# Kernel optimization log

Measured on AMD Instinct MI355X. Metric: run time of the kernel, lower is better.

Reference implementation:

```python
import jax, jax.numpy as jnp
import numpy as np

DIM_V = 512
H = 8
EPS = 1e-5

def _layernorm(x, g, b):
    mu = jnp.mean(x, axis=-1, keepdims=True)
    var = jnp.var(x, axis=-1, keepdims=True)
    return (x - mu) * jax.lax.rsqrt(var + EPS) * g + b

def setup_inputs() -> dict:
    key = jax.random.key(0)
    ks = jax.random.split(key, 10)
    B, Nq, Nk, dq, dk, dv = 8, 1024, 1024, 512, 512, DIM_V
    def lin(k, fan_in, shape):
        bound = 1.0 / np.sqrt(fan_in)
        return jax.random.uniform(k, shape, jnp.float32, -bound, bound)
    return {
        "Q": jax.random.normal(ks[0], (B, Nq, dq), jnp.float32),
        "K": jax.random.normal(ks[1], (B, Nk, dk), jnp.float32),
        "Wq": lin(ks[2], dq, (dv, dq)), "bq": lin(ks[3], dq, (dv,)),
        "Wk": lin(ks[4], dk, (dv, dk)), "bk": lin(ks[5], dk, (dv,)),
        "Wv": lin(ks[6], dk, (dv, dk)), "bv": lin(ks[7], dk, (dv,)),
        "Wo": lin(ks[8], dv, (dv, dv)), "bo": lin(ks[9], dv, (dv,)),
        "g0": jnp.ones((dv,), jnp.float32), "beta0": jnp.zeros((dv,), jnp.float32),
        "g1": jnp.ones((dv,), jnp.float32), "beta1": jnp.zeros((dv,), jnp.float32),
    }

def reference(Q, K, Wq, bq, Wk, bk, Wv, bv, Wo, bo, g0, beta0, g1, beta1):
    B, Nq, _ = Q.shape
    Nk = K.shape[1]
    d_h = DIM_V // H
    Qp = Q @ Wq.T + bq            # [B,Nq,dv]
    Kp = K @ Wk.T + bk            # [B,Nk,dv]
    Vp = K @ Wv.T + bv            # [B,Nk,dv]
    # split heads along feature dim (matches torch split(dim_split,2)+cat(0))
    Qh = Qp.reshape(B, Nq, H, d_h).transpose(0, 2, 1, 3)  # [B,H,Nq,dh]
    Kh = Kp.reshape(B, Nk, H, d_h).transpose(0, 2, 1, 3)
    Vh = Vp.reshape(B, Nk, H, d_h).transpose(0, 2, 1, 3)
    # NOTE: original scales by sqrt(dim_V), the FULL model dim
    scores = jnp.einsum('bhnd,bhmd->bhnm', Qh, Kh) / jnp.sqrt(jnp.float32(DIM_V))
    A = jax.nn.softmax(scores, axis=-1)                   # [B,H,Nq,Nk]
    Oh = Qh + jnp.einsum('bhnm,bhmd->bhnd', A, Vh)        # residual on projected Q
    O = Oh.transpose(0, 2, 1, 3).reshape(B, Nq, DIM_V)
    O = _layernorm(O, g0, beta0)
    O = O + jax.nn.relu(O @ Wo.T + bo)
    O = _layernorm(O, g1, beta1)
    return O
```

## Files before the change

### kernel.cpp

```cpp
#include <hip/hip_runtime.h>
#include <hip/hip_bf16.h>

typedef __hip_bfloat16 bf16;
typedef short bf16x8 __attribute__((ext_vector_type(8)));
typedef float f32x4 __attribute__((ext_vector_type(4)));
typedef unsigned int u32;

static __device__ __forceinline__ float bfu2f(unsigned short u) { return __uint_as_float((u32)u << 16); }
static __device__ __forceinline__ u32 pack2(float a, float b) {
    return (u32)__bfloat16_as_ushort(__float2bfloat16(a))
         | ((u32)__bfloat16_as_ushort(__float2bfloat16(b)) << 16);
}
static __device__ __forceinline__ float wave_sum(float v) {
    #pragma unroll
    for (int off = 32; off > 0; off >>= 1) v += __shfl_xor(v, off);
    return v;
}

static __device__ __forceinline__ void gll16(const bf16* g, bf16* l) {
    __builtin_amdgcn_global_load_lds((const __attribute__((address_space(1))) void*)g,
                                     (__attribute__((address_space(3))) void*)l,
                                     16, 0, 0);
}

__global__ __launch_bounds__(256) void castall(const float* __restrict__ Q,  const float* __restrict__ K,
                                               const float* __restrict__ Wq, const float* __restrict__ Wk,
                                               const float* __restrict__ Wv, const float* __restrict__ Wo,
                                               bf16* __restrict__ dQ,  bf16* __restrict__ dK,
                                               bf16* __restrict__ dWq, bf16* __restrict__ dWk,
                                               bf16* __restrict__ dWv, bf16* __restrict__ dWo)
{
    const int b = blockIdx.x;
    const float* src; bf16* dst; size_t off;
    if (b < 1024)      { src = Q;  dst = dQ;  off = (size_t)b * 4096; }
    else if (b < 2048) { src = K;  dst = dK;  off = (size_t)(b - 1024) * 4096; }
    else {
        const int wb = b - 2048, wi = wb >> 6;
        off = (size_t)(wb & 63) * 4096;
        src = wi == 0 ? Wq : wi == 1 ? Wk : wi == 2 ? Wv : Wo;
        dst = wi == 0 ? dWq : wi == 1 ? dWk : wi == 2 ? dWv : dWo;
    }
    const size_t p = off + threadIdx.x * 16;
    const float4 v0 = *(const float4*)(src + p);
    const float4 v1 = *(const float4*)(src + p + 4);
    const float4 v2 = *(const float4*)(src + p + 8);
    const float4 v3 = *(const float4*)(src + p + 12);
    uint4 o0, o1;
    o0.x = pack2(v0.x, v0.y); o0.y = pack2(v0.z, v0.w);
    o0.z = pack2(v1.x, v1.y); o0.w = pack2(v1.z, v1.w);
    o1.x = pack2(v2.x, v2.y); o1.y = pack2(v2.z, v2.w);
    o1.z = pack2(v3.x, v3.y); o1.w = pack2(v3.z, v3.w);
    *(uint4*)(dst + p)     = o0;
    *(uint4*)(dst + p + 8) = o1;
}

__global__ __launch_bounds__(256) void gemm_qkv(const bf16* __restrict__ Aq, const bf16* __restrict__ Ak,
                                                const bf16* __restrict__ Wq, const bf16* __restrict__ Wk,
                                                const bf16* __restrict__ Wv,
                                                const float* __restrict__ bq, const float* __restrict__ bk,
                                                const float* __restrict__ bv,
                                                bf16* __restrict__ oQ, bf16* __restrict__ oK,
                                                bf16* __restrict__ oV)
{
    __shared__ bf16 As[128 * 32];
    __shared__ bf16 Bs[128 * 32];

    const int tid = threadIdx.x, lane = tid & 63, wave = tid >> 6;
    const int yy = blockIdx.y, wi = yy >> 2;
    const bf16* A     = wi == 0 ? Aq : Ak;
    const bf16* W     = wi == 0 ? Wq : wi == 1 ? Wk : Wv;
    const float* bias = wi == 0 ? bq : wi == 1 ? bk : bv;
    bf16* out         = wi == 0 ? oQ : wi == 1 ? oK : oV;
    const int mode    = wi == 2 ? 2 : 1;
    const int bm = blockIdx.x * 128;
    const int bn = (yy & 3) * 128;

    const int srow = tid >> 2;
    const int sg8  = (((tid & 3) ^ (srow & 3)) * 8);
    const int wm = (wave >> 1) * 64, wn = (wave & 1) * 64;
    const int fr = lane & 15, fq = lane >> 4;
    const int kqs = ((fq ^ (fr & 3)) * 8);

    f32x4 acc[4][4] = {};
    const bf16* Ap = A + (size_t)(bm + srow) * 512 + sg8;
    const bf16* Wp = W + (size_t)(bn + srow) * 512 + sg8;
    bf16* AsD = As + 8 * tid;
    bf16* BsD = Bs + 8 * tid;

    for (int k0 = 0; k0 < 512; k0 += 32) {
        __syncthreads();
        gll16(Ap + k0,                    AsD);
        gll16(Ap + k0 + (size_t)64 * 512, AsD + 2048);
        gll16(Wp + k0,                    BsD);
        gll16(Wp + k0 + (size_t)64 * 512, BsD + 2048);
        __syncthreads();

        bf16x8 fa[4], fb[4];
        #pragma unroll
        for (int i = 0; i < 4; i++) {
            fa[i] = *(const bf16x8*)(&As[(wm + 16 * i + fr) * 32 + kqs]);
            fb[i] = *(const bf16x8*)(&Bs[(wn + 16 * i + fr) * 32 + kqs]);
        }
        #pragma unroll
        for (int i = 0; i < 4; i++)
            #pragma unroll
            for (int j = 0; j < 4; j++)
                acc[i][j] = __builtin_amdgcn_mfma_f32_16x16x32_bf16(fa[i], fb[j], acc[i][j], 0, 0, 0);
    }

    const int r0 = fq * 4;
    #pragma unroll
    for (int i = 0; i < 4; i++) {
        #pragma unroll
        for (int j = 0; j < 4; j++) {
            const int col = bn + wn + 16 * j + fr;
            const float bv2 = bias[col];
            #pragma unroll
            for (int r = 0; r < 4; r++) {
                const int row = bm + wm + 16 * i + r0 + r;
                const float v = acc[i][j][r] + bv2;
                const int b = row >> 10, n = row & 1023;
                const int h = col >> 6,  d = col & 63;
                size_t idx;
                if (mode == 1) idx = ((size_t)(b * 8 + h) * 1024 + n) * 64 + d;
                else           idx = ((size_t)(b * 8 + h) * 64 + d) * 1024 + n;
                out[idx] = __float2bfloat16(v);
            }
        }
    }
}

__global__ __launch_bounds__(256) void gemm_o(const bf16* __restrict__ A,
                                              const bf16* __restrict__ W,
                                              const float* __restrict__ bias,
                                              bf16* __restrict__ out)
{
    __shared__ bf16 As[64 * 32];
    __shared__ bf16 Bs[128 * 32];

    const int tid = threadIdx.x, lane = tid & 63, wave = tid >> 6;
    const int bm = blockIdx.x * 64;
    const int bn = blockIdx.y * 128;

    const int srow = tid >> 2;
    const int sg8  = (((tid & 3) ^ (srow & 3)) * 8);
    const int wn = wave * 32;
    const int fr = lane & 15, fq = lane >> 4;
    const int kqs = ((fq ^ (fr & 3)) * 8);

    f32x4 acc[4][2] = {};
    const bf16* Ap = A + (size_t)(bm + srow) * 512 + sg8;
    const bf16* Wp = W + (size_t)(bn + srow) * 512 + sg8;
    bf16* AsD = As + 8 * tid;
    bf16* BsD = Bs + 8 * tid;

    for (int k0 = 0; k0 < 512; k0 += 32) {
        __syncthreads();
        gll16(Ap + k0,                    AsD);
        gll16(Wp + k0,                    BsD);
        gll16(Wp + k0 + (size_t)64 * 512, BsD + 2048);
        __syncthreads();

        bf16x8 fa[4], fb[2];
        #pragma unroll
        for (int i = 0; i < 4; i++)
            fa[i] = *(const bf16x8*)(&As[(16 * i + fr) * 32 + kqs]);
        #pragma unroll
        for (int j = 0; j < 2; j++)
            fb[j] = *(const bf16x8*)(&Bs[(wn + 16 * j + fr) * 32 + kqs]);
        #pragma unroll
        for (int i = 0; i < 4; i++)
            #pragma unroll
            for (int j = 0; j < 2; j++)
                acc[i][j] = __builtin_amdgcn_mfma_f32_16x16x32_bf16(fa[i], fb[j], acc[i][j], 0, 0, 0);
    }

    const int r0 = fq * 4;
    #pragma unroll
    for (int i = 0; i < 4; i++) {
        #pragma unroll
        for (int j = 0; j < 2; j++) {
            const int col = bn + wn + 16 * j + fr;
            const float bv = bias[col];
            #pragma unroll
            for (int r = 0; r < 4; r++) {
                const int row = bm + 16 * i + r0 + r;
                out[(size_t)row * 512 + col] = __float2bfloat16(acc[i][j][r] + bv);
            }
        }
    }
}

__global__ __launch_bounds__(256) void attn_mfma(const bf16* __restrict__ Qh,
                                                 const bf16* __restrict__ Kh,
                                                 const bf16* __restrict__ VhT,
                                                 bf16* __restrict__ Oc)
{
    __shared__ bf16 Ks[64 * 64];
    __shared__ bf16 Vs[64 * 64];
    __shared__ bf16 Ps[4][16 * 72];

    const int tid = threadIdx.x, lane = tid & 63, w = tid >> 6;
    const int bh = blockIdx.y;
    const int wq = blockIdx.x * 64 + w * 16;

    const bf16* Qb = Qh  + ((size_t)bh * 1024 + wq) * 64;
    const bf16* Kb = Kh  + (size_t)bh * 1024 * 64;
    const bf16* Vb = VhT + (size_t)bh * 64 * 1024;

    const int fl = lane & 15, fq = lane >> 4;
    const int flk = fl & 7;
    const int gA = (fq ^ flk) * 8;
    const int gB = ((4 | fq) ^ flk) * 8;

    bf16x8 qf0 = *(const bf16x8*)(Qb + fl * 64 + fq * 8);
    bf16x8 qf1 = *(const bf16x8*)(Qb + fl * 64 + 32 + fq * 8);

    f32x4 o[4] = {};
    float lsum = 0.f;
    const float sc2 = 0.04419417382415922f * 1.4426950408889634f;

    const int srow = tid >> 3;
    const int sg8  = (((tid & 7) ^ (srow & 7)) * 8);
    const bf16* KbR = Kb + (size_t)srow * 64 + sg8;
    const bf16* VbR0 = Vb + (size_t)srow * 1024 + sg8;
    const bf16* VbR1 = Vb + (size_t)(srow + 32) * 1024 + sg8;
    bf16* KsD = Ks + 8 * tid;
    bf16* VsD = Vs + 8 * tid;

    for (int kt = 0; kt < 16; kt++) {
        const int m0 = kt * 64;
        __syncthreads();
        gll16(KbR + (size_t)m0 * 64,        KsD);
        gll16(KbR + (size_t)(m0 + 32) * 64, KsD + 2048);
        gll16(VbR0 + m0,                    VsD);
        gll16(VbR1 + m0,                    VsD + 2048);
        __syncthreads();

        f32x4 st[4] = {};
        #pragma unroll
        for (int tm = 0; tm < 4; tm++) {
            bf16x8 kf0 = *(const bf16x8*)(&Ks[(16 * tm + fl) * 64 + gA]);
            bf16x8 kf1 = *(const bf16x8*)(&Ks[(16 * tm + fl) * 64 + gB]);
            st[tm] = __builtin_amdgcn_mfma_f32_16x16x32_bf16(kf0, qf0, st[tm], 0, 0, 0);
            st[tm] = __builtin_amdgcn_mfma_f32_16x16x32_bf16(kf1, qf1, st[tm], 0, 0, 0);
        }

        #pragma unroll
        for (int tm = 0; tm < 4; tm++) {
            float p0 = __builtin_amdgcn_exp2f(st[tm][0] * sc2);
            float p1 = __builtin_amdgcn_exp2f(st[tm][1] * sc2);
            float p2 = __builtin_amdgcn_exp2f(st[tm][2] * sc2);
            float p3 = __builtin_amdgcn_exp2f(st[tm][3] * sc2);
            lsum += (p0 + p1) + (p2 + p3);
            uint2 pk;
            pk.x = pack2(p0, p1);
            pk.y = pack2(p2, p3);
            *(uint2*)(&Ps[w][fl * 72 + 16 * tm + fq * 4]) = pk;
        }

        bf16x8 pf0 = *(const bf16x8*)(&Ps[w][fl * 72 + fq * 8]);
        bf16x8 pf1 = *(const bf16x8*)(&Ps[w][fl * 72 + 32 + fq * 8]);
        #pragma unroll
        for (int jd = 0; jd < 4; jd++) {
            bf16x8 vf0 = *(const bf16x8*)(&Vs[(16 * jd + fl) * 64 + gA]);
            bf16x8 vf1 = *(const bf16x8*)(&Vs[(16 * jd + fl) * 64 + gB]);
            o[jd] = __builtin_amdgcn_mfma_f32_16x16x32_bf16(vf0, pf0, o[jd], 0, 0, 0);
            o[jd] = __builtin_amdgcn_mfma_f32_16x16x32_bf16(vf1, pf1, o[jd], 0, 0, 0);
        }
    }

    lsum += __shfl_xor(lsum, 16);
    lsum += __shfl_xor(lsum, 32);
    const float linv = 1.f / lsum;

    const int b = bh >> 3, h = bh & 7;
    const size_t obase = ((size_t)(b * 1024 + wq + fl)) * 512 + h * 64;
    #pragma unroll
    for (int jd = 0; jd < 4; jd++) {
        const ushort4 qr = *(const ushort4*)(Qb + fl * 64 + 16 * jd + fq * 4);
        const float v0 = o[jd][0] * linv + bfu2f(qr.x);
        const float v1 = o[jd][1] * linv + bfu2f(qr.y);
        const float v2 = o[jd][2] * linv + bfu2f(qr.z);
        const float v3 = o[jd][3] * linv + bfu2f(qr.w);
        uint2 w2;
        w2.x = pack2(v0, v1);
        w2.y = pack2(v2, v3);
        *(uint2*)(&Oc[obase + 16 * jd + fq * 4]) = w2;
    }
}

__global__ __launch_bounds__(256) void ln0(const bf16* __restrict__ X,
                                           const float* __restrict__ g,
                                           const float* __restrict__ be,
                                           bf16* __restrict__ Y)
{
    const int lane = threadIdx.x & 63;
    const int row = blockIdx.x * 4 + (threadIdx.x >> 6);
    const size_t base = (size_t)row * 512 + lane * 8;
    const bf16x8 xv = *(const bf16x8*)(X + base);
    float x[8];
    #pragma unroll
    for (int j = 0; j < 8; j++) x[j] = bfu2f((unsigned short)xv[j]);
    float s = 0.f, s2 = 0.f;
    #pragma unroll
    for (int j = 0; j < 8; j++) { s += x[j]; s2 += x[j] * x[j]; }
    s = wave_sum(s); s2 = wave_sum(s2);
    const float mean = s * (1.f / 512.f);
    const float var = s2 * (1.f / 512.f) - mean * mean;
    const float rs = rsqrtf(fmaxf(var, 0.f) + 1e-5f);
    const float4 gv0 = *(const float4*)(g + lane * 8);
    const float4 gv1 = *(const float4*)(g + lane * 8 + 4);
    const float4 bv0 = *(const float4*)(be + lane * 8);
    const float4 bv1 = *(const float4*)(be + lane * 8 + 4);
    uint4 ov;
    ov.x = pack2((x[0]-mean)*rs*gv0.x + bv0.x, (x[1]-mean)*rs*gv0.y + bv0.y);
    ov.y = pack2((x[2]-mean)*rs*gv0.z + bv0.z, (x[3]-mean)*rs*gv0.w + bv0.w);
    ov.z = pack2((x[4]-mean)*rs*gv1.x + bv1.x, (x[5]-mean)*rs*gv1.y + bv1.y);
    ov.w = pack2((x[6]-mean)*rs*gv1.z + bv1.z, (x[7]-mean)*rs*gv1.w + bv1.w);
    *(uint4*)(Y + base) = ov;
}

__global__ __launch_bounds__(256) void ln1(const bf16* __restrict__ X,
                                           const bf16* __restrict__ R,
                                           const float* __restrict__ g,
                                           const float* __restrict__ be,
                                           float* __restrict__ Y)
{
    const int lane = threadIdx.x & 63;
    const int row = blockIdx.x * 4 + (threadIdx.x >> 6);
    const size_t base = (size_t)row * 512 + lane * 8;
    const bf16x8 xv = *(const bf16x8*)(X + base);
    const bf16x8 rv = *(const bf16x8*)(R + base);
    float x[8];
    #pragma unroll
    for (int j = 0; j < 8; j++)
        x[j] = bfu2f((unsigned short)rv[j]) + fmaxf(bfu2f((unsigned short)xv[j]), 0.f);
    float s = 0.f, s2 = 0.f;
    #pragma unroll
    for (int j = 0; j < 8; j++) { s += x[j]; s2 += x[j] * x[j]; }
    s = wave_sum(s); s2 = wave_sum(s2);
    const float mean = s * (1.f / 512.f);
    const float var = s2 * (1.f / 512.f) - mean * mean;
    const float rs = rsqrtf(fmaxf(var, 0.f) + 1e-5f);
    const float4 gv0 = *(const float4*)(g + lane * 8);
    const float4 gv1 = *(const float4*)(g + lane * 8 + 4);
    const float4 bv0 = *(const float4*)(be + lane * 8);
    const float4 bv1 = *(const float4*)(be + lane * 8 + 4);
    float4 y0, y1;
    y0.x = (x[0]-mean)*rs*gv0.x + bv0.x; y0.y = (x[1]-mean)*rs*gv0.y + bv0.y;
    y0.z = (x[2]-mean)*rs*gv0.z + bv0.z; y0.w = (x[3]-mean)*rs*gv0.w + bv0.w;
    y1.x = (x[4]-mean)*rs*gv1.x + bv1.x; y1.y = (x[5]-mean)*rs*gv1.y + bv1.y;
    y1.z = (x[6]-mean)*rs*gv1.z + bv1.z; y1.w = (x[7]-mean)*rs*gv1.w + bv1.w;
    *(float4*)(Y + base)     = y0;
    *(float4*)(Y + base + 4) = y1;
}

extern "C" void kernel_launch(void* const* d_in, const int* in_sizes, int n_in,
                              void* d_out, int out_size, void* d_ws, size_t ws_size,
                              hipStream_t stream)
{
    const float* Q   = (const float*)d_in[0];
    const float* K   = (const float*)d_in[1];
    const float* Wq  = (const float*)d_in[2];
    const float* bq  = (const float*)d_in[3];
    const float* Wk  = (const float*)d_in[4];
    const float* bk  = (const float*)d_in[5];
    const float* Wv  = (const float*)d_in[6];
    const float* bv  = (const float*)d_in[7];
    const float* Wo  = (const float*)d_in[8];
    const float* bo  = (const float*)d_in[9];
    const float* g0  = (const float*)d_in[10];
    const float* be0 = (const float*)d_in[11];
    const float* g1  = (const float*)d_in[12];
    const float* be1 = (const float*)d_in[13];
    float* out = (float*)d_out;

    const size_t NQK = (size_t)8 * 1024 * 512;
    const size_t NW  = (size_t)512 * 512;
    bf16* ws   = (bf16*)d_ws;
    bf16* cQ   = ws;
    bf16* cK   = cQ + NQK;
    bf16* cWq  = cK + NQK;
    bf16* cWk  = cWq + NW;
    bf16* cWv  = cWk + NW;
    bf16* cWo  = cWv + NW;
    bf16* pQh  = cWo + NW;
    bf16* pKh  = pQh + NQK;
    bf16* pVhT = pKh + NQK;
    bf16* pOc  = (bf16*)d_out;
    bf16* pO1  = pKh;
    bf16* pTmp = pQh;

    castall<<<2304, 256, 0, stream>>>(Q, K, Wq, Wk, Wv, Wo, cQ, cK, cWq, cWk, cWv, cWo);
    gemm_qkv<<<dim3(64, 12), 256, 0, stream>>>(cQ, cK, cWq, cWk, cWv, bq, bk, bv, pQh, pKh, pVhT);
    attn_mfma<<<dim3(16, 64), 256, 0, stream>>>(pQh, pKh, pVhT, pOc);
    ln0<<<2048, 256, 0, stream>>>(pOc, g0, be0, pO1);
    gemm_o<<<dim3(128, 4), 256, 0, stream>>>(pO1, cWo, bo, pTmp);
    ln1<<<2048, 256, 0, stream>>>(pTmp, pO1, g1, be1, out);
}
```

Before: 189.1 us.

## Double-buffer LDS tiles in QKV, output-projection and attention kernels

```diff
diff --git a/kernel.cpp b/kernel.cpp
--- a/kernel.cpp
+++ b/kernel.cpp
@@ -62,8 +62,8 @@
                                                 bf16* __restrict__ oQ, bf16* __restrict__ oK,
                                                 bf16* __restrict__ oV)
 {
-    __shared__ bf16 As[128 * 32];
-    __shared__ bf16 Bs[128 * 32];
+    __shared__ bf16 As[2][128 * 32];
+    __shared__ bf16 Bs[2][128 * 32];
 
     const int tid = threadIdx.x, lane = tid & 63, wave = tid >> 6;
     const int yy = blockIdx.y, wi = yy >> 2;
@@ -84,28 +84,35 @@
     f32x4 acc[4][4] = {};
     const bf16* Ap = A + (size_t)(bm + srow) * 512 + sg8;
     const bf16* Wp = W + (size_t)(bn + srow) * 512 + sg8;
-    bf16* AsD = As + 8 * tid;
-    bf16* BsD = Bs + 8 * tid;
-
+    const int ld = 8 * tid;
+
+    gll16(Ap,                    As[0] + ld);
+    gll16(Ap + (size_t)64 * 512, As[0] + 2048 + ld);
+    gll16(Wp,                    Bs[0] + ld);
+    gll16(Wp + (size_t)64 * 512, Bs[0] + 2048 + ld);
+
+    int cur = 0;
     for (int k0 = 0; k0 < 512; k0 += 32) {
         __syncthreads();
-        gll16(Ap + k0,                    AsD);
-        gll16(Ap + k0 + (size_t)64 * 512, AsD + 2048);
-        gll16(Wp + k0,                    BsD);
-        gll16(Wp + k0 + (size_t)64 * 512, BsD + 2048);
-        __syncthreads();
-
+        if (k0 + 32 < 512) {
+            const int nxt = cur ^ 1;
+            gll16(Ap + k0 + 32,                    As[nxt] + ld);
+            gll16(Ap + k0 + 32 + (size_t)64 * 512, As[nxt] + 2048 + ld);
+            gll16(Wp + k0 + 32,                    Bs[nxt] + ld);
+            gll16(Wp + k0 + 32 + (size_t)64 * 512, Bs[nxt] + 2048 + ld);
+        }
         bf16x8 fa[4], fb[4];
         #pragma unroll
         for (int i = 0; i < 4; i++) {
-            fa[i] = *(const bf16x8*)(&As[(wm + 16 * i + fr) * 32 + kqs]);
-            fb[i] = *(const bf16x8*)(&Bs[(wn + 16 * i + fr) * 32 + kqs]);
+            fa[i] = *(const bf16x8*)(&As[cur][(wm + 16 * i + fr) * 32 + kqs]);
+            fb[i] = *(const bf16x8*)(&Bs[cur][(wn + 16 * i + fr) * 32 + kqs]);
         }
         #pragma unroll
         for (int i = 0; i < 4; i++)
             #pragma unroll
             for (int j = 0; j < 4; j++)
                 acc[i][j] = __builtin_amdgcn_mfma_f32_16x16x32_bf16(fa[i], fb[j], acc[i][j], 0, 0, 0);
+        cur ^= 1;
     }
 
     const int r0 = fq * 4;
@@ -135,8 +142,8 @@
                                               const float* __restrict__ bias,
                                               bf16* __restrict__ out)
 {
-    __shared__ bf16 As[64 * 32];
-    __shared__ bf16 Bs[128 * 32];
+    __shared__ bf16 As[2][64 * 32];
+    __shared__ bf16 Bs[2][128 * 32];
 
     const int tid = threadIdx.x, lane = tid & 63, wave = tid >> 6;
     const int bm = blockIdx.x * 64;
@@ -151,28 +158,34 @@
     f32x4 acc[4][2] = {};
     const bf16* Ap = A + (size_t)(bm + srow) * 512 + sg8;
     const bf16* Wp = W + (size_t)(bn + srow) * 512 + sg8;
-    bf16* AsD = As + 8 * tid;
-    bf16* BsD = Bs + 8 * tid;
-
+    const int ld = 8 * tid;
+
+    gll16(Ap,                    As[0] + ld);
+    gll16(Wp,                    Bs[0] + ld);
+    gll16(Wp + (size_t)64 * 512, Bs[0] + 2048 + ld);
+
+    int cur = 0;
     for (int k0 = 0; k0 < 512; k0 += 32) {
         __syncthreads();
-        gll16(Ap + k0,                    AsD);
-        gll16(Wp + k0,                    BsD);
-        gll16(Wp + k0 + (size_t)64 * 512, BsD + 2048);
-        __syncthreads();
-
+        if (k0 + 32 < 512) {
+            const int nxt = cur ^ 1;
+            gll16(Ap + k0 + 32,                    As[nxt] + ld);
+            gll16(Wp + k0 + 32,                    Bs[nxt] + ld);
+            gll16(Wp + k0 + 32 + (size_t)64 * 512, Bs[nxt] + 2048 + ld);
+        }
         bf16x8 fa[4], fb[2];
         #pragma unroll
         for (int i = 0; i < 4; i++)
-            fa[i] = *(const bf16x8*)(&As[(16 * i + fr) * 32 + kqs]);
+            fa[i] = *(const bf16x8*)(&As[cur][(16 * i + fr) * 32 + kqs]);
         #pragma unroll
         for (int j = 0; j < 2; j++)
-            fb[j] = *(const bf16x8*)(&Bs[(wn + 16 * j + fr) * 32 + kqs]);
+            fb[j] = *(const bf16x8*)(&Bs[cur][(wn + 16 * j + fr) * 32 + kqs]);
         #pragma unroll
         for (int i = 0; i < 4; i++)
             #pragma unroll
             for (int j = 0; j < 2; j++)
                 acc[i][j] = __builtin_amdgcn_mfma_f32_16x16x32_bf16(fa[i], fb[j], acc[i][j], 0, 0, 0);
+        cur ^= 1;
     }
 
     const int r0 = fq * 4;
@@ -196,8 +209,8 @@
                                                  const bf16* __restrict__ VhT,
                                                  bf16* __restrict__ Oc)
 {
-    __shared__ bf16 Ks[64 * 64];
-    __shared__ bf16 Vs[64 * 64];
+    __shared__ bf16 Ks[2][64 * 64];
+    __shared__ bf16 Vs[2][64 * 64];
     __shared__ bf16 Ps[4][16 * 72];
 
     const int tid = threadIdx.x, lane = tid & 63, w = tid >> 6;
@@ -222,26 +235,33 @@
 
     const int srow = tid >> 3;
     const int sg8  = (((tid & 7) ^ (srow & 7)) * 8);
-    const bf16* KbR = Kb + (size_t)srow * 64 + sg8;
+    const bf16* KbR  = Kb + (size_t)srow * 64 + sg8;
     const bf16* VbR0 = Vb + (size_t)srow * 1024 + sg8;
     const bf16* VbR1 = Vb + (size_t)(srow + 32) * 1024 + sg8;
-    bf16* KsD = Ks + 8 * tid;
-    bf16* VsD = Vs + 8 * tid;
-
+    const int ld = 8 * tid;
+
+    gll16(KbR,               Ks[0] + ld);
+    gll16(KbR + 32 * 64,     Ks[0] + 2048 + ld);
+    gll16(VbR0,              Vs[0] + ld);
+    gll16(VbR1,              Vs[0] + 2048 + ld);
+
+    int cur = 0;
     for (int kt = 0; kt < 16; kt++) {
-        const int m0 = kt * 64;
         __syncthreads();
-        gll16(KbR + (size_t)m0 * 64,        KsD);
-        gll16(KbR + (size_t)(m0 + 32) * 64, KsD + 2048);
-        gll16(VbR0 + m0,                    VsD);
-        gll16(VbR1 + m0,                    VsD + 2048);
-        __syncthreads();
+        if (kt < 15) {
+            const int nxt = cur ^ 1;
+            const int m1 = (kt + 1) * 64;
+            gll16(KbR + (size_t)m1 * 64,        Ks[nxt] + ld);
+            gll16(KbR + (size_t)(m1 + 32) * 64, Ks[nxt] + 2048 + ld);
+            gll16(VbR0 + m1,                    Vs[nxt] + ld);
+            gll16(VbR1 + m1,                    Vs[nxt] + 2048 + ld);
+        }
 
         f32x4 st[4] = {};
         #pragma unroll
         for (int tm = 0; tm < 4; tm++) {
-            bf16x8 kf0 = *(const bf16x8*)(&Ks[(16 * tm + fl) * 64 + gA]);
-            bf16x8 kf1 = *(const bf16x8*)(&Ks[(16 * tm + fl) * 64 + gB]);
+            bf16x8 kf0 = *(const bf16x8*)(&Ks[cur][(16 * tm + fl) * 64 + gA]);
+            bf16x8 kf1 = *(const bf16x8*)(&Ks[cur][(16 * tm + fl) * 64 + gB]);
             st[tm] = __builtin_amdgcn_mfma_f32_16x16x32_bf16(kf0, qf0, st[tm], 0, 0, 0);
             st[tm] = __builtin_amdgcn_mfma_f32_16x16x32_bf16(kf1, qf1, st[tm], 0, 0, 0);
         }
@@ -263,11 +283,12 @@
         bf16x8 pf1 = *(const bf16x8*)(&Ps[w][fl * 72 + 32 + fq * 8]);
         #pragma unroll
         for (int jd = 0; jd < 4; jd++) {
-            bf16x8 vf0 = *(const bf16x8*)(&Vs[(16 * jd + fl) * 64 + gA]);
-            bf16x8 vf1 = *(const bf16x8*)(&Vs[(16 * jd + fl) * 64 + gB]);
+            bf16x8 vf0 = *(const bf16x8*)(&Vs[cur][(16 * jd + fl) * 64 + gA]);
+            bf16x8 vf1 = *(const bf16x8*)(&Vs[cur][(16 * jd + fl) * 64 + gB]);
             o[jd] = __builtin_amdgcn_mfma_f32_16x16x32_bf16(vf0, pf0, o[jd], 0, 0, 0);
             o[jd] = __builtin_amdgcn_mfma_f32_16x16x32_bf16(vf1, pf1, o[jd], 0, 0, 0);
         }
+        cur ^= 1;
     }
 
     lsum += __shfl_xor(lsum, 16);
```

Result: slower. 196.1 us (+3.7%).

## Drop LDS staging in GEMMs and attention, load MFMA fragments directly from global

Applied to the files above, without the earlier changes.

```diff
diff --git a/kernel.cpp b/kernel.cpp
--- a/kernel.cpp
+++ b/kernel.cpp
@@ -15,12 +15,6 @@
     #pragma unroll
     for (int off = 32; off > 0; off >>= 1) v += __shfl_xor(v, off);
     return v;
-}
-
-static __device__ __forceinline__ void gll16(const bf16* g, bf16* l) {
-    __builtin_amdgcn_global_load_lds((const __attribute__((address_space(1))) void*)g,
-                                     (__attribute__((address_space(3))) void*)l,
-                                     16, 0, 0);
 }
 
 __global__ __launch_bounds__(256) void castall(const float* __restrict__ Q,  const float* __restrict__ K,
@@ -62,9 +56,6 @@
                                                 bf16* __restrict__ oQ, bf16* __restrict__ oK,
                                                 bf16* __restrict__ oV)
 {
-    __shared__ bf16 As[128 * 32];
-    __shared__ bf16 Bs[128 * 32];
-
     const int tid = threadIdx.x, lane = tid & 63, wave = tid >> 6;
     const int yy = blockIdx.y, wi = yy >> 2;
     const bf16* A     = wi == 0 ? Aq : Ak;
@@ -75,31 +66,20 @@
     const int bm = blockIdx.x * 128;
     const int bn = (yy & 3) * 128;
 
-    const int srow = tid >> 2;
-    const int sg8  = (((tid & 3) ^ (srow & 3)) * 8);
     const int wm = (wave >> 1) * 64, wn = (wave & 1) * 64;
     const int fr = lane & 15, fq = lane >> 4;
-    const int kqs = ((fq ^ (fr & 3)) * 8);
 
     f32x4 acc[4][4] = {};
-    const bf16* Ap = A + (size_t)(bm + srow) * 512 + sg8;
-    const bf16* Wp = W + (size_t)(bn + srow) * 512 + sg8;
-    bf16* AsD = As + 8 * tid;
-    bf16* BsD = Bs + 8 * tid;
-
+    const bf16* Ap = A + (size_t)(bm + wm + fr) * 512 + fq * 8;
+    const bf16* Wp = W + (size_t)(bn + wn + fr) * 512 + fq * 8;
+
+    #pragma unroll 2
     for (int k0 = 0; k0 < 512; k0 += 32) {
-        __syncthreads();
-        gll16(Ap + k0,                    AsD);
-        gll16(Ap + k0 + (size_t)64 * 512, AsD + 2048);
-        gll16(Wp + k0,                    BsD);
-        gll16(Wp + k0 + (size_t)64 * 512, BsD + 2048);
-        __syncthreads();
-
         bf16x8 fa[4], fb[4];
         #pragma unroll
         for (int i = 0; i < 4; i++) {
-            fa[i] = *(const bf16x8*)(&As[(wm + 16 * i + fr) * 32 + kqs]);
-            fb[i] = *(const bf16x8*)(&Bs[(wn + 16 * i + fr) * 32 + kqs]);
+            fa[i] = *(const bf16x8*)(Ap + (size_t)(16 * i) * 512 + k0);
+            fb[i] = *(const bf16x8*)(Wp + (size_t)(16 * i) * 512 + k0);
         }
         #pragma unroll
         for (int i = 0; i < 4; i++)
@@ -135,39 +115,25 @@
                                               const float* __restrict__ bias,
                                               bf16* __restrict__ out)
 {
-    __shared__ bf16 As[64 * 32];
-    __shared__ bf16 Bs[128 * 32];
-
     const int tid = threadIdx.x, lane = tid & 63, wave = tid >> 6;
     const int bm = blockIdx.x * 64;
     const int bn = blockIdx.y * 128;
-
-    const int srow = tid >> 2;
-    const int sg8  = (((tid & 3) ^ (srow & 3)) * 8);
     const int wn = wave * 32;
     const int fr = lane & 15, fq = lane >> 4;
-    const int kqs = ((fq ^ (fr & 3)) * 8);
 
     f32x4 acc[4][2] = {};
-    const bf16* Ap = A + (size_t)(bm + srow) * 512 + sg8;
-    const bf16* Wp = W + (size_t)(bn + srow) * 512 + sg8;
-    bf16* AsD = As + 8 * tid;
-    bf16* BsD = Bs + 8 * tid;
-
+    const bf16* Ap = A + (size_t)(bm + fr) * 512 + fq * 8;
+    const bf16* Wp = W + (size_t)(bn + wn + fr) * 512 + fq * 8;
+
+    #pragma unroll 2
     for (int k0 = 0; k0 < 512; k0 += 32) {
-        __syncthreads();
-        gll16(Ap + k0,                    AsD);
-        gll16(Wp + k0,                    BsD);
-        gll16(Wp + k0 + (size_t)64 * 512, BsD + 2048);
-        __syncthreads();
-
         bf16x8 fa[4], fb[2];
         #pragma unroll
         for (int i = 0; i < 4; i++)
-            fa[i] = *(const bf16x8*)(&As[(16 * i + fr) * 32 + kqs]);
+            fa[i] = *(const bf16x8*)(Ap + (size_t)(16 * i) * 512 + k0);
         #pragma unroll
         for (int j = 0; j < 2; j++)
-            fb[j] = *(const bf16x8*)(&Bs[(wn + 16 * j + fr) * 32 + kqs]);
+            fb[j] = *(const bf16x8*)(Wp + (size_t)(16 * j) * 512 + k0);
         #pragma unroll
         for (int i = 0; i < 4; i++)
             #pragma unroll
@@ -196,22 +162,18 @@
                                                  const bf16* __restrict__ VhT,
                                                  bf16* __restrict__ Oc)
 {
-    __shared__ bf16 Ks[64 * 64];
-    __shared__ bf16 Vs[64 * 64];
     __shared__ bf16 Ps[4][16 * 72];
 
     const int tid = threadIdx.x, lane = tid & 63, w = tid >> 6;
-    const int bh = blockIdx.y;
-    const int wq = blockIdx.x * 64 + w * 16;
+    const int id = blockIdx.x;
+    const int bh = (id & 7) * 8 + (id >> 7);
+    const int wq = ((id >> 3) & 15) * 64 + w * 16;
 
     const bf16* Qb = Qh  + ((size_t)bh * 1024 + wq) * 64;
     const bf16* Kb = Kh  + (size_t)bh * 1024 * 64;
     const bf16* Vb = VhT + (size_t)bh * 64 * 1024;
 
     const int fl = lane & 15, fq = lane >> 4;
-    const int flk = fl & 7;
-    const int gA = (fq ^ flk) * 8;
-    const int gB = ((4 | fq) ^ flk) * 8;
 
     bf16x8 qf0 = *(const bf16x8*)(Qb + fl * 64 + fq * 8);
     bf16x8 qf1 = *(const bf16x8*)(Qb + fl * 64 + 32 + fq * 8);
@@ -220,30 +182,32 @@
     float lsum = 0.f;
     const float sc2 = 0.04419417382415922f * 1.4426950408889634f;
 
-    const int srow = tid >> 3;
-    const int sg8  = (((tid & 7) ^ (srow & 7)) * 8);
-    const bf16* KbR = Kb + (size_t)srow * 64 + sg8;
-    const bf16* VbR0 = Vb + (size_t)srow * 1024 + sg8;
-    const bf16* VbR1 = Vb + (size_t)(srow + 32) * 1024 + sg8;
-    bf16* KsD = Ks + 8 * tid;
-    bf16* VsD = Vs + 8 * tid;
+    const bf16* KpA = Kb + (size_t)fl * 64 + fq * 8;
+    const bf16* VpA = Vb + (size_t)fl * 1024 + fq * 8;
 
     for (int kt = 0; kt < 16; kt++) {
         const int m0 = kt * 64;
-        __syncthreads();
-        gll16(KbR + (size_t)m0 * 64,        KsD);
-        gll16(KbR + (size_t)(m0 + 32) * 64, KsD + 2048);
-        gll16(VbR0 + m0,                    VsD);
-        gll16(VbR1 + m0,                    VsD + 2048);
-        __syncthreads();
-
+
+        bf16x8 kf[4][2];
+        #pragma unroll
+        for (int tm = 0; tm < 4; tm++) {
+            const bf16* p = KpA + (size_t)(m0 + 16 * tm) * 64;
+            kf[tm][0] = *(const bf16x8*)(p);
+            kf[tm][1] = *(const bf16x8*)(p + 32);
+        }
         f32x4 st[4] = {};
         #pragma unroll
         for (int tm = 0; tm < 4; tm++) {
-            bf16x8 kf0 = *(const bf16x8*)(&Ks[(16 * tm + fl) * 64 + gA]);
-            bf16x8 kf1 = *(const bf16x8*)(&Ks[(16 * tm + fl) * 64 + gB]);
-            st[tm] = __builtin_amdgcn_mfma_f32_16x16x32_bf16(kf0, qf0, st[tm], 0, 0, 0);
-            st[tm] = __builtin_amdgcn_mfma_f32_16x16x32_bf16(kf1, qf1, st[tm], 0, 0, 0);
+            st[tm] = __builtin_amdgcn_mfma_f32_16x16x32_bf16(kf[tm][0], qf0, st[tm], 0, 0, 0);
+            st[tm] = __builtin_amdgcn_mfma_f32_16x16x32_bf16(kf[tm][1], qf1, st[tm], 0, 0, 0);
+        }
+
+        bf16x8 vf[4][2];
+        #pragma unroll
+        for (int jd = 0; jd < 4; jd++) {
+            const bf16* p = VpA + (size_t)(16 * jd) * 1024 + m0;
+            vf[jd][0] = *(const bf16x8*)(p);
+            vf[jd][1] = *(const bf16x8*)(p + 32);
         }
 
         #pragma unroll
@@ -263,10 +227,8 @@
         bf16x8 pf1 = *(const bf16x8*)(&Ps[w][fl * 72 + 32 + fq * 8]);
         #pragma unroll
         for (int jd = 0; jd < 4; jd++) {
-            bf16x8 vf0 = *(const bf16x8*)(&Vs[(16 * jd + fl) * 64 + gA]);
-            bf16x8 vf1 = *(const bf16x8*)(&Vs[(16 * jd + fl) * 64 + gB]);
-            o[jd] = __builtin_amdgcn_mfma_f32_16x16x32_bf16(vf0, pf0, o[jd], 0, 0, 0);
-            o[jd] = __builtin_amdgcn_mfma_f32_16x16x32_bf16(vf1, pf1, o[jd], 0, 0, 0);
+            o[jd] = __builtin_amdgcn_mfma_f32_16x16x32_bf16(vf[jd][0], pf0, o[jd], 0, 0, 0);
+            o[jd] = __builtin_amdgcn_mfma_f32_16x16x32_bf16(vf[jd][1], pf1, o[jd], 0, 0, 0);
         }
     }
 
@@ -394,7 +356,7 @@
 
     castall<<<2304, 256, 0, stream>>>(Q, K, Wq, Wk, Wv, Wo, cQ, cK, cWq, cWk, cWv, cWo);
     gemm_qkv<<<dim3(64, 12), 256, 0, stream>>>(cQ, cK, cWq, cWk, cWv, bq, bk, bv, pQh, pKh, pVhT);
-    attn_mfma<<<dim3(16, 64), 256, 0, stream>>>(pQh, pKh, pVhT, pOc);
+    attn_mfma<<<1024, 256, 0, stream>>>(pQh, pKh, pVhT, pOc);
     ln0<<<2048, 256, 0, stream>>>(pOc, g0, be0, pO1);
     gemm_o<<<dim3(128, 4), 256, 0, stream>>>(pO1, cWo, bo, pTmp);
     ln1<<<2048, 256, 0, stream>>>(pTmp, pO1, g1, be1, out);
```

New measurement: 316.3 us. 67.3% more time.
